# Optimization experiments

Hardware: AMD Instinct MI355X
Metric: run time of the kernel (lower is better)

Reference implementation:

```python
import jax, jax.numpy as jnp
import numpy as np

EMBED = 256
HEADS = 8
LEVELS = 1
POINTS = 4
NBQ = 2          # num_bev_queue
HBEV = 128
WBEV = 128
BS = 1


def setup_inputs() -> dict:
    key = jax.random.key(0)
    ks = jax.random.split(key, 10)
    Nq = HBEV * WBEV
    E = EMBED
    so_out = NBQ * HEADS * LEVELS * POINTS * 2
    aw_out = NBQ * HEADS * LEVELS * POINTS
    return {
        "query": jax.random.normal(ks[0], (BS, Nq, E), jnp.float32),
        "value": jax.random.normal(ks[1], (BS, NBQ * Nq, E), jnp.float32),
        "reference_points": jax.random.uniform(ks[2], (BS, Nq, LEVELS, 2), jnp.float32),
        # params stored as [in, out]; y = x @ W + b (math-equivalent to torch Linear)
        "W_vproj": jax.random.normal(ks[3], (E, E), jnp.float32) / np.sqrt(E).astype(np.float32),
        "b_vproj": jnp.zeros((E,), jnp.float32),
        "W_so": jax.random.normal(ks[4], (NBQ * E, so_out), jnp.float32) * 0.01,
        "b_so": jax.random.normal(ks[5], (so_out,), jnp.float32) * 0.5,
        "W_aw": jax.random.normal(ks[6], (NBQ * E, aw_out), jnp.float32) * 0.01,
        "b_aw": jnp.zeros((aw_out,), jnp.float32),
        "W_out": jax.random.normal(ks[7], (E, E), jnp.float32) / np.sqrt(E).astype(np.float32),
        "b_out": jnp.zeros((E,), jnp.float32),
        "spatial_shapes": jnp.array([[HBEV, WBEV]], jnp.int32),
        "level_start_index": jnp.array([0], jnp.int32),
    }


def _msda(value, spatial_shapes, sampling_locations, attention_weights):
    """Multi-scale deformable attention (grid_sample semantics: bilinear,
    zero padding, align_corners=False).
    value: [B, sum(H*W), Hh, d]; sampling_locations: [B, Nq, Hh, L, P, 2] in [0,1];
    attention_weights: [B, Nq, Hh, L, P]. Returns [B, Nq, Hh*d]."""
    B, _, Hh, d = value.shape
    _, Nq, _, L, P, _ = sampling_locations.shape
    ss = np.asarray(spatial_shapes)
    out = jnp.zeros((B, Nq, Hh, d), value.dtype)
    start = 0
    for l in range(L):
        H_, W_ = int(ss[l, 0]), int(ss[l, 1])
        v = value[:, start:start + H_ * W_]          # [B, H*W, Hh, d]
        start += H_ * W_
        loc = sampling_locations[:, :, :, l]          # [B, Nq, Hh, P, 2]
        # align_corners=False: pixel = loc*size - 0.5
        px = loc[..., 0] * W_ - 0.5
        py = loc[..., 1] * H_ - 0.5
        x0f = jnp.floor(px)
        y0f = jnp.floor(py)
        lx = px - x0f
        ly = py - y0f
        x0 = x0f.astype(jnp.int32)
        y0 = y0f.astype(jnp.int32)

        def gather(ix, iy):
            valid = ((ix >= 0) & (ix < W_) & (iy >= 0) & (iy < H_))
            idx = jnp.clip(iy, 0, H_ - 1) * W_ + jnp.clip(ix, 0, W_ - 1)   # [B,Nq,Hh,P]
            idx = jnp.transpose(idx, (0, 1, 3, 2)).reshape(B, Nq * P, Hh, 1)
            g = jnp.take_along_axis(v, idx, axis=1).reshape(B, Nq, P, Hh, d)
            m = jnp.transpose(valid, (0, 1, 3, 2))[..., None].astype(value.dtype)
            return g * m

        def wmul(w):  # [B,Nq,Hh,P] -> [B,Nq,P,Hh,1]
            return jnp.transpose(w, (0, 1, 3, 2))[..., None]

        sampled = (wmul((1 - lx) * (1 - ly)) * gather(x0, y0)
                   + wmul(lx * (1 - ly)) * gather(x0 + 1, y0)
                   + wmul((1 - lx) * ly) * gather(x0, y0 + 1)
                   + wmul(lx * ly) * gather(x0 + 1, y0 + 1))   # [B,Nq,P,Hh,d]
        out = out + jnp.einsum('bqphd,bqhp->bqhd', sampled, attention_weights[:, :, :, l])
    return out.reshape(B, Nq, Hh * d)


def reference(query, value, reference_points, W_vproj, b_vproj, W_so, b_so,
              W_aw, b_aw, W_out, b_out, spatial_shapes, level_start_index):
    bs, Nq, E = query.shape
    Hh, L, P, nbq = HEADS, LEVELS, POINTS, NBQ
    identity = query
    # query enhanced with the previous-BEV slice of value
    qe = jnp.concatenate([value[:, :Nq], query], axis=-1)        # [bs, Nq, 2E]
    v = (value @ W_vproj + b_vproj).reshape(bs * nbq, Nq, Hh, E // Hh)
    so = (qe @ W_so + b_so).reshape(bs, Nq, Hh, nbq, L, P, 2)
    aw = jax.nn.softmax((qe @ W_aw + b_aw).reshape(bs, Nq, Hh, nbq, L * P), axis=-1)
    aw = aw.reshape(bs, Nq, Hh, nbq, L, P)
    aw = jnp.transpose(aw, (0, 3, 1, 2, 4, 5)).reshape(bs * nbq, Nq, Hh, L, P)
    so = jnp.transpose(so, (0, 3, 1, 2, 4, 5, 6)).reshape(bs * nbq, Nq, Hh, L, P, 2)
    rp = jnp.tile(reference_points, (nbq, 1, 1, 1))              # [bs*nbq, Nq, L, 2]
    ssf = spatial_shapes.astype(so.dtype)
    offset_normalizer = jnp.stack([ssf[:, 1], ssf[:, 0]], -1)    # [L, 2] = (W, H)
    loc = rp[:, :, None, :, None, :] + so / offset_normalizer[None, None, None, :, None, :]
    out = _msda(v, spatial_shapes, loc, aw).reshape(bs, nbq, Nq, E).mean(axis=1)
    out = out @ W_out + b_out
    return out + identity  # dropout is identity in eval mode
```

## Files before the change

kernel.cpp:

```cpp
#include <hip/hip_runtime.h>
#include <math.h>

#define NQ     16384
#define NHEAD  8
#define GW     128
#define GH     128

typedef __attribute__((ext_vector_type(8))) short short8;
typedef __attribute__((ext_vector_type(4))) float f32x4;

static __device__ __forceinline__ unsigned short f2bf(float f) {
    unsigned u = __builtin_bit_cast(unsigned, f);
    u += 0x7FFFu + ((u >> 16) & 1u);
    return (unsigned short)(u >> 16);
}
static __device__ __forceinline__ unsigned pk2(float lo, float hi) {
    return (unsigned)f2bf(lo) | ((unsigned)f2bf(hi) << 16);
}
static __device__ __forceinline__ float bflo(unsigned u) {
    return __builtin_bit_cast(float, u << 16);
}
static __device__ __forceinline__ float bfhi(unsigned u) {
    return __builtin_bit_cast(float, u & 0xffff0000u);
}

__global__ void prep(const float* __restrict__ Wv, const float* __restrict__ Wso,
                     const float* __restrict__ Waw, const float* __restrict__ bso,
                     const float* __restrict__ baw, const float* __restrict__ Wo,
                     unsigned short* __restrict__ WTv, unsigned short* __restrict__ WTso,
                     unsigned short* __restrict__ WTo, float* __restrict__ bias2)
{
    const int n = blockIdx.x;
    const int k = threadIdx.x;
    WTv[n * 256 + k] = f2bf(Wv[(size_t)k * 256 + n]);
    WTo[n * 256 + k] = f2bf(Wo[(size_t)k * 256 + n]);
    float s0, s1;
    if (n < 128)      { s0 = Wso[(size_t)k * 128 + n];       s1 = Wso[(size_t)(k + 256) * 128 + n]; }
    else if (n < 192) { s0 = Waw[(size_t)k * 64 + n - 128];  s1 = Waw[(size_t)(k + 256) * 64 + n - 128]; }
    else              { s0 = 0.f; s1 = 0.f; }
    WTso[(size_t)n * 512 + k]       = f2bf(s0);
    WTso[(size_t)n * 512 + k + 256] = f2bf(s1);
    if (k == 0) bias2[n] = (n < 128) ? bso[n] : ((n < 192) ? baw[n - 128] : 0.f);
}

template<int KTOT, int MODE>
static __device__ __forceinline__ void gemm_body(
    int m0, int n0,
    const float* __restrict__ A1, const float* __restrict__ A2,
    const unsigned short* __restrict__ Abf,
    const unsigned short* __restrict__ WT,
    const float* __restrict__ bias, const float* __restrict__ resid,
    void* __restrict__ Cout,
    unsigned short* As, unsigned short* Bs)
{
    const int tid = threadIdx.x;
    const int w = tid >> 6, lane = tid & 63;
    const int wr = w >> 1, wc = w & 1;
    const int g = lane >> 4, r16 = lane & 15;

    f32x4 acc[4][4] = {};

    for (int k0 = 0; k0 < KTOT; k0 += 64) {
        if (MODE == 2) {
            #pragma unroll
            for (int c = 0; c < 4; ++c) {
                int idx = tid + c * 256;
                int row = idx >> 3, oct = idx & 7;
                uint4 wv = *reinterpret_cast<const uint4*>(
                    &Abf[(size_t)(m0 + row) * 256 + k0 + oct * 8]);
                *reinterpret_cast<uint4*>(&As[(oct * 128 + row) * 8]) = wv;
            }
        } else {
            const float* Asrc = (KTOT == 512 && k0 >= 256) ? (A2 + (k0 - 256)) : (A1 + k0);
            #pragma unroll
            for (int c = 0; c < 4; ++c) {
                int idx = tid + c * 256;
                int row = idx >> 3, oct = idx & 7;
                const float* p = Asrc + (size_t)(m0 + row) * 256 + oct * 8;
                float4 f0 = *reinterpret_cast<const float4*>(p);
                float4 f1 = *reinterpret_cast<const float4*>(p + 4);
                uint4 wv;
                wv.x = pk2(f0.x, f0.y); wv.y = pk2(f0.z, f0.w);
                wv.z = pk2(f1.x, f1.y); wv.w = pk2(f1.z, f1.w);
                *reinterpret_cast<uint4*>(&As[(oct * 128 + row) * 8]) = wv;
            }
        }
        #pragma unroll
        for (int c = 0; c < 4; ++c) {
            int idx = tid + c * 256;
            int n = idx >> 3, oct = idx & 7;
            uint4 wv = *reinterpret_cast<const uint4*>(
                &WT[(size_t)(n0 + n) * KTOT + k0 + oct * 8]);
            *reinterpret_cast<uint4*>(&Bs[(oct * 128 + n) * 8]) = wv;
        }
        __syncthreads();

        #pragma unroll
        for (int kh = 0; kh < 2; ++kh) {
            short8 af[4], bfr[4];
            #pragma unroll
            for (int m = 0; m < 4; ++m)
                af[m] = *reinterpret_cast<const short8*>(
                    &As[(((kh * 4 + g) * 128) + wr * 64 + m * 16 + r16) * 8]);
            #pragma unroll
            for (int n = 0; n < 4; ++n)
                bfr[n] = *reinterpret_cast<const short8*>(
                    &Bs[(((kh * 4 + g) * 128) + wc * 64 + n * 16 + r16) * 8]);
            #pragma unroll
            for (int m = 0; m < 4; ++m)
                #pragma unroll
                for (int n = 0; n < 4; ++n)
                    acc[m][n] = __builtin_amdgcn_mfma_f32_16x16x32_bf16(
                        af[m], bfr[n], acc[m][n], 0, 0, 0);
        }
        __syncthreads();
    }

    #pragma unroll
    for (int m = 0; m < 4; ++m) {
        int row = m0 + wr * 64 + m * 16 + g * 4;
        #pragma unroll
        for (int n = 0; n < 4; ++n) {
            int col = n0 + wc * 64 + n * 16 + r16;
            if (MODE == 1 && col >= 192) continue;
            float bia = bias[col];
            #pragma unroll
            for (int j = 0; j < 4; ++j) {
                float vo = acc[m][n][j] + bia;
                if (MODE == 0) {
                    ((unsigned short*)Cout)[(size_t)(row + j) * 256 + col] = f2bf(vo);
                } else if (MODE == 1) {
                    ((float*)Cout)[(size_t)(row + j) * 192 + col] = vo;
                } else {
                    ((float*)Cout)[(size_t)(row + j) * 256 + col] =
                        vo + resid[(size_t)(row + j) * 256 + col];
                }
            }
        }
    }
}

__global__ __launch_bounds__(256, 2)
void gemm_vs(const float* __restrict__ value, const float* __restrict__ query,
             const unsigned short* __restrict__ WTv, const unsigned short* __restrict__ WTso,
             const float* __restrict__ bv, const float* __restrict__ bias2,
             unsigned short* __restrict__ v_out, float* __restrict__ soaw_out)
{
    __shared__ __align__(16) unsigned short As[8 * 128 * 8];
    __shared__ __align__(16) unsigned short Bs[8 * 128 * 8];
    const int bid = blockIdx.x;
    if (bid < 512) {
        gemm_body<256, 0>((bid >> 1) * 128, (bid & 1) * 128,
                          value, nullptr, nullptr, WTv, bv, nullptr, v_out, As, Bs);
    } else {
        const int b2 = bid - 512;
        gemm_body<512, 1>((b2 >> 1) * 128, (b2 & 1) * 128,
                          value, query, nullptr, WTso, bias2, nullptr, soaw_out, As, Bs);
    }
}

__global__ __launch_bounds__(256, 2)
void gemm_out(const unsigned short* __restrict__ Abf, const unsigned short* __restrict__ WTo,
              const float* __restrict__ bo, const float* __restrict__ resid,
              float* __restrict__ out)
{
    __shared__ __align__(16) unsigned short As[8 * 128 * 8];
    __shared__ __align__(16) unsigned short Bs[8 * 128 * 8];
    const int bid = blockIdx.x;
    gemm_body<256, 2>((bid >> 1) * 128, (bid & 1) * 128,
                      nullptr, nullptr, Abf, WTo, bo, resid, out, As, Bs);
}

static __device__ __forceinline__ void acc8(float* acc, float w, uint4 r) {
    acc[0] = fmaf(w, bflo(r.x), acc[0]);
    acc[1] = fmaf(w, bfhi(r.x), acc[1]);
    acc[2] = fmaf(w, bflo(r.y), acc[2]);
    acc[3] = fmaf(w, bfhi(r.y), acc[3]);
    acc[4] = fmaf(w, bflo(r.z), acc[4]);
    acc[5] = fmaf(w, bfhi(r.z), acc[5]);
    acc[6] = fmaf(w, bflo(r.w), acc[6]);
    acc[7] = fmaf(w, bfhi(r.w), acc[7]);
}

__global__ __launch_bounds__(256)
void sampler(const unsigned short* __restrict__ v, const float* __restrict__ soaw,
             const float* __restrict__ rp, unsigned short* __restrict__ outm)
{
    __shared__ float so_s[8][128];
    __shared__ float w_s[8][64];
    __shared__ float rp_s[8][2];

    const int t = threadIdx.x;
    const int bid = blockIdx.x;
    const int q0 = ((bid & 7) * 256 + (bid >> 3)) * 8;

    #pragma unroll
    for (int i = 0; i < 4; ++i) {
        int idx = t + i * 256;
        int qq = idx >> 7, off = idx & 127;
        so_s[qq][off] = soaw[(size_t)(q0 + qq) * 192 + off];
    }
    if (t < 128) {
        int qq = t >> 4, grp = t & 15;
        float4 a4 = *reinterpret_cast<const float4*>(
            &soaw[(size_t)(q0 + qq) * 192 + 128 + grp * 4]);
        float m = fmaxf(fmaxf(a4.x, a4.y), fmaxf(a4.z, a4.w));
        float e0 = __expf(a4.x - m), e1 = __expf(a4.y - m);
        float e2 = __expf(a4.z - m), e3 = __expf(a4.w - m);
        float inv = 1.f / (e0 + e1 + e2 + e3);
        w_s[qq][grp * 4 + 0] = e0 * inv;
        w_s[qq][grp * 4 + 1] = e1 * inv;
        w_s[qq][grp * 4 + 2] = e2 * inv;
        w_s[qq][grp * 4 + 3] = e3 * inv;
    }
    if (t < 16) rp_s[t >> 1][t & 1] = rp[(size_t)(q0 + (t >> 1)) * 2 + (t & 1)];
    __syncthreads();

    const int wq = t >> 5;
    const int q = q0 + wq;
    const int s = t & 31;
    const int h = s >> 2, c = s & 3;
    const int sub = h * 64 + c * 16;
    const float rpx = rp_s[wq][0], rpy = rp_s[wq][1];
    float acc[8] = {};

    #pragma unroll
    for (int b = 0; b < 2; ++b) {
        const char* vb = (const char*)v + (size_t)b * NQ * 512;
        #pragma unroll
        for (int p = 0; p < 4; ++p) {
            float sox = so_s[wq][h * 16 + b * 8 + p * 2 + 0];
            float soy = so_s[wq][h * 16 + b * 8 + p * 2 + 1];
            float wbp = w_s[wq][h * 8 + b * 4 + p];
            float px = (rpx + sox * (1.0f / 128.0f)) * 128.0f - 0.5f;
            float py = (rpy + soy * (1.0f / 128.0f)) * 128.0f - 0.5f;
            float x0f = floorf(px), y0f = floorf(py);
            float lx = px - x0f, ly = py - y0f;
            int x0 = (int)x0f, y0 = (int)y0f;
            int x1 = x0 + 1, y1 = y0 + 1;
            float wx0 = (1.f - lx) * ((x0 >= 0 && x0 < GW) ? 1.f : 0.f);
            float wx1 = lx         * ((x1 >= 0 && x1 < GW) ? 1.f : 0.f);
            float wy0 = (1.f - ly) * ((y0 >= 0 && y0 < GH) ? 1.f : 0.f);
            float wy1 = ly         * ((y1 >= 0 && y1 < GH) ? 1.f : 0.f);
            int x0c = min(max(x0, 0), GW - 1), x1c = min(max(x1, 0), GW - 1);
            int y0c = min(max(y0, 0), GH - 1), y1c = min(max(y1, 0), GH - 1);
            uint4 r00 = *(const uint4*)(vb + ((size_t)(y0c * GW + x0c) * 512 + sub));
            uint4 r10 = *(const uint4*)(vb + ((size_t)(y0c * GW + x1c) * 512 + sub));
            uint4 r01 = *(const uint4*)(vb + ((size_t)(y1c * GW + x0c) * 512 + sub));
            uint4 r11 = *(const uint4*)(vb + ((size_t)(y1c * GW + x1c) * 512 + sub));
            acc8(acc, wbp * wx0 * wy0, r00);
            acc8(acc, wbp * wx1 * wy0, r10);
            acc8(acc, wbp * wx0 * wy1, r01);
            acc8(acc, wbp * wx1 * wy1, r11);
        }
    }

    uint4 o;
    o.x = pk2(0.5f * acc[0], 0.5f * acc[1]);
    o.y = pk2(0.5f * acc[2], 0.5f * acc[3]);
    o.z = pk2(0.5f * acc[4], 0.5f * acc[5]);
    o.w = pk2(0.5f * acc[6], 0.5f * acc[7]);
    *reinterpret_cast<uint4*>((char*)outm + (size_t)q * 512 + sub) = o;
}

extern "C" void kernel_launch(void* const* d_in, const int* in_sizes, int n_in,
                              void* d_out, int out_size, void* d_ws, size_t ws_size,
                              hipStream_t stream)
{
    const float* query   = (const float*)d_in[0];
    const float* value   = (const float*)d_in[1];
    const float* rp      = (const float*)d_in[2];
    const float* W_vproj = (const float*)d_in[3];
    const float* b_vproj = (const float*)d_in[4];
    const float* W_so    = (const float*)d_in[5];
    const float* b_so    = (const float*)d_in[6];
    const float* W_aw    = (const float*)d_in[7];
    const float* b_aw    = (const float*)d_in[8];
    const float* W_out   = (const float*)d_in[9];
    const float* b_out   = (const float*)d_in[10];
    float* out = (float*)d_out;

    char* wp = (char*)d_ws;
    unsigned short* ws_v    = (unsigned short*)wp; wp += (size_t)2 * NQ * 256 * 2;
    float*          ws_soaw = (float*)wp;          wp += (size_t)NQ * 192 * 4;
    unsigned short* ws_mean = (unsigned short*)wp; wp += (size_t)NQ * 256 * 2;
    unsigned short* WTv     = (unsigned short*)wp; wp += 256 * 256 * 2;
    unsigned short* WTso    = (unsigned short*)wp; wp += 256 * 512 * 2;
    unsigned short* WTo     = (unsigned short*)wp; wp += 256 * 256 * 2;
    float*          bias2   = (float*)wp;          wp += 256 * 4;

    prep<<<dim3(256), dim3(256), 0, stream>>>(W_vproj, W_so, W_aw, b_so, b_aw, W_out,
                                              WTv, WTso, WTo, bias2);
    gemm_vs<<<dim3(768), dim3(256), 0, stream>>>(value, query, WTv, WTso,
                                                 b_vproj, bias2, ws_v, ws_soaw);
    sampler<<<dim3(NQ / 8), dim3(256), 0, stream>>>(ws_v, ws_soaw, rp, ws_mean);
    gemm_out<<<dim3(256), dim3(256), 0, stream>>>(ws_mean, WTo, b_out, query, out);
}
```

Measured before the change: 95.53 us.

## Double-buffer GEMM tiles with register prefetch, shrink M tile, split fused launch

Rewrites the shared GEMM body to prefetch the next K-tile into registers while MFMAs run on the current LDS buffer, using two LDS buffers and one barrier per iteration. The M tile is halved from 128 to 64 rows, which doubles the grid size for more CUs and waves. The combined vproj/soaw kernel is split into two launches. The LDS layout moves to a row-major 64-wide stride, which may cause bank conflicts. Each tile also reuses B less, and the extra launch adds overhead.

```diff
diff --git a/kernel.cpp b/kernel.cpp
--- a/kernel.cpp
+++ b/kernel.cpp
@@ -57,76 +57,106 @@
     const int w = tid >> 6, lane = tid & 63;
     const int wr = w >> 1, wc = w & 1;
     const int g = lane >> 4, r16 = lane & 15;
-
-    f32x4 acc[4][4] = {};
-
-    for (int k0 = 0; k0 < KTOT; k0 += 64) {
-        if (MODE == 2) {
-            #pragma unroll
-            for (int c = 0; c < 4; ++c) {
-                int idx = tid + c * 256;
-                int row = idx >> 3, oct = idx & 7;
-                uint4 wv = *reinterpret_cast<const uint4*>(
-                    &Abf[(size_t)(m0 + row) * 256 + k0 + oct * 8]);
-                *reinterpret_cast<uint4*>(&As[(oct * 128 + row) * 8]) = wv;
-            }
-        } else {
-            const float* Asrc = (KTOT == 512 && k0 >= 256) ? (A2 + (k0 - 256)) : (A1 + k0);
-            #pragma unroll
-            for (int c = 0; c < 4; ++c) {
-                int idx = tid + c * 256;
-                int row = idx >> 3, oct = idx & 7;
-                const float* p = Asrc + (size_t)(m0 + row) * 256 + oct * 8;
-                float4 f0 = *reinterpret_cast<const float4*>(p);
-                float4 f1 = *reinterpret_cast<const float4*>(p + 4);
-                uint4 wv;
-                wv.x = pk2(f0.x, f0.y); wv.y = pk2(f0.z, f0.w);
-                wv.z = pk2(f1.x, f1.y); wv.w = pk2(f1.z, f1.w);
-                *reinterpret_cast<uint4*>(&As[(oct * 128 + row) * 8]) = wv;
-            }
-        }
-        #pragma unroll
-        for (int c = 0; c < 4; ++c) {
-            int idx = tid + c * 256;
-            int n = idx >> 3, oct = idx & 7;
-            uint4 wv = *reinterpret_cast<const uint4*>(
-                &WT[(size_t)(n0 + n) * KTOT + k0 + oct * 8]);
-            *reinterpret_cast<uint4*>(&Bs[(oct * 128 + n) * 8]) = wv;
-        }
-        __syncthreads();
-
+    const int arow = tid >> 3, aoc = tid & 7;
+    const int NT = KTOT / 64;
+
+    float4 ra[4];
+    uint4  rab[2];
+    uint4  rb[4];
+    f32x4 acc[2][4] = {};
+
+#define LOAD_T(t)                                                               \
+    {                                                                           \
+        int k0 = (t) * 64;                                                      \
+        if (MODE == 2) {                                                        \
+            _Pragma("unroll")                                                   \
+            for (int i = 0; i < 2; ++i)                                         \
+                rab[i] = *(const uint4*)&Abf[(size_t)(m0 + arow + i * 32) * 256 \
+                                             + k0 + aoc * 8];                   \
+        } else {                                                                \
+            const float* Asrc = (KTOT == 512 && k0 >= 256) ? (A2 + (k0 - 256))  \
+                                                           : (A1 + k0);         \
+            _Pragma("unroll")                                                   \
+            for (int i = 0; i < 2; ++i) {                                       \
+                const float* p = Asrc + (size_t)(m0 + arow + i * 32) * 256      \
+                                 + aoc * 8;                                     \
+                ra[i * 2 + 0] = *(const float4*)p;                              \
+                ra[i * 2 + 1] = *(const float4*)(p + 4);                        \
+            }                                                                   \
+        }                                                                       \
+        _Pragma("unroll")                                                       \
+        for (int i = 0; i < 4; ++i)                                             \
+            rb[i] = *(const uint4*)&WT[(size_t)(n0 + arow + i * 32) * KTOT      \
+                                       + k0 + aoc * 8];                         \
+    }
+
+#define WRITE_T(bufi)                                                           \
+    {                                                                           \
+        unsigned short* Ab = As + (bufi) * 64 * 64;                             \
+        unsigned short* Bb = Bs + (bufi) * 128 * 64;                            \
+        if (MODE == 2) {                                                        \
+            _Pragma("unroll")                                                   \
+            for (int i = 0; i < 2; ++i)                                         \
+                *(uint4*)&Ab[(arow + i * 32) * 64 + aoc * 8] = rab[i];          \
+        } else {                                                                \
+            _Pragma("unroll")                                                   \
+            for (int i = 0; i < 2; ++i) {                                       \
+                uint4 wv;                                                       \
+                wv.x = pk2(ra[i * 2].x, ra[i * 2].y);                           \
+                wv.y = pk2(ra[i * 2].z, ra[i * 2].w);                           \
+                wv.z = pk2(ra[i * 2 + 1].x, ra[i * 2 + 1].y);                   \
+                wv.w = pk2(ra[i * 2 + 1].z, ra[i * 2 + 1].w);                   \
+                *(uint4*)&Ab[(arow + i * 32) * 64 + aoc * 8] = wv;              \
+            }                                                                   \
+        }                                                                       \
+        _Pragma("unroll")                                                       \
+        for (int i = 0; i < 4; ++i)                                             \
+            *(uint4*)&Bb[(arow + i * 32) * 64 + aoc * 8] = rb[i];               \
+    }
+
+    LOAD_T(0);
+    WRITE_T(0);
+    __syncthreads();
+
+    for (int t = 0; t < NT; ++t) {
+        if (t + 1 < NT) LOAD_T(t + 1);
+        const unsigned short* Ab = As + (t & 1) * 64 * 64;
+        const unsigned short* Bb = Bs + (t & 1) * 128 * 64;
         #pragma unroll
         for (int kh = 0; kh < 2; ++kh) {
-            short8 af[4], bfr[4];
+            short8 af[2], bfr[4];
             #pragma unroll
-            for (int m = 0; m < 4; ++m)
-                af[m] = *reinterpret_cast<const short8*>(
-                    &As[(((kh * 4 + g) * 128) + wr * 64 + m * 16 + r16) * 8]);
+            for (int mi = 0; mi < 2; ++mi)
+                af[mi] = *(const short8*)&Ab[(wr * 32 + mi * 16 + r16) * 64
+                                             + (kh * 4 + g) * 8];
             #pragma unroll
-            for (int n = 0; n < 4; ++n)
-                bfr[n] = *reinterpret_cast<const short8*>(
-                    &Bs[(((kh * 4 + g) * 128) + wc * 64 + n * 16 + r16) * 8]);
+            for (int nj = 0; nj < 4; ++nj)
+                bfr[nj] = *(const short8*)&Bb[(wc * 64 + nj * 16 + r16) * 64
+                                              + (kh * 4 + g) * 8];
             #pragma unroll
-            for (int m = 0; m < 4; ++m)
+            for (int mi = 0; mi < 2; ++mi)
                 #pragma unroll
-                for (int n = 0; n < 4; ++n)
-                    acc[m][n] = __builtin_amdgcn_mfma_f32_16x16x32_bf16(
-                        af[m], bfr[n], acc[m][n], 0, 0, 0);
+                for (int nj = 0; nj < 4; ++nj)
+                    acc[mi][nj] = __builtin_amdgcn_mfma_f32_16x16x32_bf16(
+                        af[mi], bfr[nj], acc[mi][nj], 0, 0, 0);
         }
+        if (t + 1 < NT) WRITE_T((t + 1) & 1);
         __syncthreads();
     }
+#undef LOAD_T
+#undef WRITE_T
 
     #pragma unroll
-    for (int m = 0; m < 4; ++m) {
-        int row = m0 + wr * 64 + m * 16 + g * 4;
+    for (int mi = 0; mi < 2; ++mi) {
+        int row = m0 + wr * 32 + mi * 16 + g * 4;
         #pragma unroll
-        for (int n = 0; n < 4; ++n) {
-            int col = n0 + wc * 64 + n * 16 + r16;
+        for (int nj = 0; nj < 4; ++nj) {
+            int col = n0 + wc * 64 + nj * 16 + r16;
             if (MODE == 1 && col >= 192) continue;
             float bia = bias[col];
             #pragma unroll
             for (int j = 0; j < 4; ++j) {
-                float vo = acc[m][n][j] + bia;
+                float vo = acc[mi][nj][j] + bia;
                 if (MODE == 0) {
                     ((unsigned short*)Cout)[(size_t)(row + j) * 256 + col] = f2bf(vo);
                 } else if (MODE == 1) {
@@ -140,34 +170,35 @@
     }
 }
 
-__global__ __launch_bounds__(256, 2)
-void gemm_vs(const float* __restrict__ value, const float* __restrict__ query,
-             const unsigned short* __restrict__ WTv, const unsigned short* __restrict__ WTso,
-             const float* __restrict__ bv, const float* __restrict__ bias2,
-             unsigned short* __restrict__ v_out, float* __restrict__ soaw_out)
-{
-    __shared__ __align__(16) unsigned short As[8 * 128 * 8];
-    __shared__ __align__(16) unsigned short Bs[8 * 128 * 8];
-    const int bid = blockIdx.x;
-    if (bid < 512) {
-        gemm_body<256, 0>((bid >> 1) * 128, (bid & 1) * 128,
-                          value, nullptr, nullptr, WTv, bv, nullptr, v_out, As, Bs);
-    } else {
-        const int b2 = bid - 512;
-        gemm_body<512, 1>((b2 >> 1) * 128, (b2 & 1) * 128,
-                          value, query, nullptr, WTso, bias2, nullptr, soaw_out, As, Bs);
-    }
-}
-
-__global__ __launch_bounds__(256, 2)
+__global__ __launch_bounds__(256)
+void gemm_vproj(const float* __restrict__ value, const unsigned short* __restrict__ WTv,
+                const float* __restrict__ bv, unsigned short* __restrict__ v_out)
+{
+    __shared__ __align__(16) unsigned short As[2 * 64 * 64];
+    __shared__ __align__(16) unsigned short Bs[2 * 128 * 64];
+    gemm_body<256, 0>((blockIdx.x >> 1) * 64, (blockIdx.x & 1) * 128,
+                      value, nullptr, nullptr, WTv, bv, nullptr, v_out, As, Bs);
+}
+
+__global__ __launch_bounds__(256)
+void gemm_soaw(const float* __restrict__ value, const float* __restrict__ query,
+               const unsigned short* __restrict__ WTso, const float* __restrict__ bias2,
+               float* __restrict__ soaw_out)
+{
+    __shared__ __align__(16) unsigned short As[2 * 64 * 64];
+    __shared__ __align__(16) unsigned short Bs[2 * 128 * 64];
+    gemm_body<512, 1>((blockIdx.x >> 1) * 64, (blockIdx.x & 1) * 128,
+                      value, query, nullptr, WTso, bias2, nullptr, soaw_out, As, Bs);
+}
+
+__global__ __launch_bounds__(256)
 void gemm_out(const unsigned short* __restrict__ Abf, const unsigned short* __restrict__ WTo,
               const float* __restrict__ bo, const float* __restrict__ resid,
               float* __restrict__ out)
 {
-    __shared__ __align__(16) unsigned short As[8 * 128 * 8];
-    __shared__ __align__(16) unsigned short Bs[8 * 128 * 8];
-    const int bid = blockIdx.x;
-    gemm_body<256, 2>((bid >> 1) * 128, (bid & 1) * 128,
+    __shared__ __align__(16) unsigned short As[2 * 64 * 64];
+    __shared__ __align__(16) unsigned short Bs[2 * 128 * 64];
+    gemm_body<256, 2>((blockIdx.x >> 1) * 64, (blockIdx.x & 1) * 128,
                       nullptr, nullptr, Abf, WTo, bo, resid, out, As, Bs);
 }
 
@@ -291,8 +322,8 @@
 
     prep<<<dim3(256), dim3(256), 0, stream>>>(W_vproj, W_so, W_aw, b_so, b_aw, W_out,
                                               WTv, WTso, WTo, bias2);
-    gemm_vs<<<dim3(768), dim3(256), 0, stream>>>(value, query, WTv, WTso,
-                                                 b_vproj, bias2, ws_v, ws_soaw);
+    gemm_vproj<<<dim3(1024), dim3(256), 0, stream>>>(value, WTv, b_vproj, ws_v);
+    gemm_soaw<<<dim3(512), dim3(256), 0, stream>>>(value, query, WTso, bias2, ws_soaw);
     sampler<<<dim3(NQ / 8), dim3(256), 0, stream>>>(ws_v, ws_soaw, rp, ws_mean);
-    gemm_out<<<dim3(256), dim3(256), 0, stream>>>(ws_mean, WTo, b_out, query, out);
-}
+    gemm_out<<<dim3(512), dim3(256), 0, stream>>>(ws_mean, WTo, b_out, query, out);
+}
```

Result: faster. 83.30 us (-12.8%).
